# Optimization experiments

Measured on AMD Instinct MI355X. Metric: run time of the kernel, lower is better.

The kernel has to match this reference:

```python
import jax, jax.numpy as jnp
import numpy as np

CHUNK = 2048  # output-direction chunk size for the fused score+reduce scan


def _stereographic_normals(out_size):
    # matches torch.meshgrid default (ij indexing): v = rows, u = cols
    v, u = jnp.meshgrid(jnp.arange(out_size, dtype=jnp.float32),
                        jnp.arange(out_size, dtype=jnp.float32), indexing='ij')
    p = 4.0 * ((u + 0.5) / out_size - 0.5)
    q = -4.0 * ((v + 0.5) / out_size - 0.5)
    d = 1.0 + p ** 2 + q ** 2
    x = 2.0 * p / d
    y = 2.0 * q / d
    z = -(-1.0 + p ** 2 + q ** 2) / d
    return jnp.stack([x, y, z], axis=-1).reshape(-1, 3)  # [out_size^2, 3]


def _forward(image, normal_map, mask, kappa, out_size):
    B, C, H, W = image.shape
    N = H * W
    k = jnp.float32(kappa)
    coef = k / (2.0 * jnp.pi * (1.0 - jnp.exp(-2.0 * k)))  # vMF normalization

    V = image.reshape(B, C, N).transpose(0, 2, 1)              # [B,N,C]
    n_in = normal_map.reshape(B, 3, N).transpose(0, 2, 1)      # [B,N,3]
    w = (mask.reshape(B, N) > 0).astype(image.dtype)[..., None]  # 0/1 validity
    # fuse numerator (v^2) and denominator (v) accumulations into one pass
    Vaug = jnp.concatenate([V * w, (V ** 2) * w], axis=-1)     # [B,N,2C]

    M = _stereographic_normals(out_size)                        # [N_out,3]
    n_chunks = M.shape[0] // CHUNK
    chunks = M.reshape(n_chunks, CHUNK, 3)

    def body(carry, Mc):
        dp = jnp.einsum('bnd,cd->bnc', n_in, Mc)                # cos similarity
        f = coef * jnp.exp(-k * (1.0 - dp))                     # vMF kernel
        return carry, jnp.einsum('bnc,bnk->bck', f, Vaug)       # [B,CHUNK,2C]

    _, outs = jax.lax.scan(jax.checkpoint(body), 0.0, chunks)   # [n_chunks,B,CHUNK,2C]
    vals = outs.transpose(1, 0, 2, 3).reshape(B, out_size * out_size, 2 * C)
    s, num = vals[..., :C], vals[..., C:]
    out_pixels = num / (s + 0.001)                              # [B,N_out,C]
    return out_pixels.transpose(0, 2, 1).reshape(B, C, out_size, out_size)


def setup_inputs() -> dict:
    key = jax.random.key(0)
    k1, k2, k3 = jax.random.split(key, 3)
    B, C, H, W = 2, 3, 128, 128
    image = jax.random.uniform(k1, (B, C, H, W), dtype=jnp.float32)
    nm = jax.random.normal(k2, (B, 3, H, W), dtype=jnp.float32)
    nm = nm / jnp.linalg.norm(nm, axis=1, keepdims=True)  # unit normals
    mask = jax.random.randint(k3, (B, H, W), 0, 2).astype(jnp.int32)
    return {"image": image, "normal_map": nm, "mask": mask,
            "kappa": 100, "out_size": 256}


def reference(image, normal_map, mask, kappa, out_size):
    return _forward(image, normal_map, mask, kappa, out_size)
```

## Files before the change

### kernel.cpp

```cpp
#include <hip/hip_runtime.h>
#include <math.h>

#define B_     2
#define C_     3
#define N_     16384
#define OS_    256
#define OUT_   65536
#define NZ_    32
#define NF_    64
#define NB_    2048
#define NITEM_ 1536
#define GRIDM_ 2048
#define CAP_   16384
#define SP2_   256
#define VSTR_  264
#define TAU_   16.0f
#define LOG2E  1.44269504088896340736f
#define PI_    3.14159265358979323846f

typedef float    f32x4 __attribute__((ext_vector_type(4)));
typedef float    v2f   __attribute__((ext_vector_type(2)));
typedef _Float16 f16x8 __attribute__((ext_vector_type(8)));
typedef __fp16   h16x2 __attribute__((ext_vector_type(2)));

static __device__ __forceinline__ v2f pk_fma(v2f a, v2f b, v2f c) {
    return __builtin_elementwise_fma(a, b, c);
}

__device__ __forceinline__ int pixel_bin(float nx, float ny, float nz) {
    int zi = (int)((nz + 1.0f) * (NZ_ * 0.5f));
    zi = min(max(zi, 0), NZ_ - 1);
    float phi = atan2f(ny, nx);
    int fi = (int)((phi + PI_) * (NF_ / (2.0f * PI_)));
    fi = min(max(fi, 0), NF_ - 1);
    return zi * NF_ + fi;
}

__global__ __launch_bounds__(256) void hist_kernel(
    const float* __restrict__ nm, const int* __restrict__ mask, int* __restrict__ cnt)
{
    int idx = blockIdx.x * 256 + threadIdx.x;
    if (idx >= B_ * N_) return;
    if (mask[idx] <= 0) return;
    int b = idx / N_, n = idx - b * N_;
    const float* nb = nm + (size_t)b * 3 * N_ + n;
    int bin = pixel_bin(nb[0], nb[N_], nb[2 * N_]);
    atomicAdd(&cnt[b * NB_ + bin], 1);
}

__global__ __launch_bounds__(64) void scan_kernel(
    const int* __restrict__ cnt, int* __restrict__ binStart, int* __restrict__ off)
{
    int b = blockIdx.x;
    int lane = threadIdx.x;
    const int per = NB_ / 64;
    int base = b * NB_ + lane * per;

    int sum = 0;
#pragma unroll
    for (int i = 0; i < per; i++) sum += cnt[base + i];

    int inc = sum;
#pragma unroll
    for (int o = 1; o < 64; o <<= 1) {
        int t = __shfl_up(inc, o);
        if (lane >= o) inc += t;
    }
    int acc = inc - sum;

#pragma unroll
    for (int i = 0; i < per; i++) {
        binStart[b * (NB_ + 1) + lane * per + i] = acc;
        off[b * NB_ + lane * per + i] = acc;
        acc += cnt[base + i];
    }
    if (lane == 63) binStart[b * (NB_ + 1) + NB_] = acc;
}

__global__ __launch_bounds__(256) void scatter_plan_kernel(
    const float* __restrict__ img, const float* __restrict__ nm,
    const int* __restrict__ mask, const int* __restrict__ kappa,
    const int* __restrict__ binStart, int* __restrict__ off,
    float* __restrict__ gn, _Float16* __restrict__ gv,
    int* __restrict__ plan, int* __restrict__ tileLen)
{
    int tid = threadIdx.x;
    int bid = blockIdx.x;
    float k = (float)kappa[0];
    float k2 = k * LOG2E;

    if (bid < 128) {
        int idx = bid * 256 + tid;
        if (idx >= B_ * N_) return;
        if (mask[idx] <= 0) return;
        int b = idx / N_, n = idx - b * N_;
        const float* nb = nm + (size_t)b * 3 * N_ + n;
        float nx = nb[0], ny = nb[N_], nz = nb[2 * N_];
        int bin = pixel_bin(nx, ny, nz);
        int pos = atomicAdd(&off[b * NB_ + bin], 1);
        const float* ib = img + (size_t)b * C_ * N_ + n;
        float v0 = ib[0], v1 = ib[N_], v2 = ib[2 * N_];
        gn[((size_t)b * 3 + 0) * CAP_ + pos] = k2 * nx;
        gn[((size_t)b * 3 + 1) * CAP_ + pos] = k2 * ny;
        gn[((size_t)b * 3 + 2) * CAP_ + pos] = k2 * nz;
        _Float16* gvb = gv + (size_t)b * 6 * CAP_;
        gvb[0 * CAP_ + pos] = (_Float16)v0;
        gvb[1 * CAP_ + pos] = (_Float16)v1;
        gvb[2 * CAP_ + pos] = (_Float16)v2;
        gvb[3 * CAP_ + pos] = (_Float16)(v0 * v0);
        gvb[4 * CAP_ + pos] = (_Float16)(v1 * v1);
        gvb[5 * CAP_ + pos] = (_Float16)(v2 * v2);
        return;
    }

    __shared__ int warr[4];
    int bt = bid - 128;
    int b = bt >> 8, tile = bt & 255;
    int tu = tile & 15, tv = tile >> 4;
    int w = tid >> 6, lane = tid & 63;

    float pc  = 4.0f * ((tu * 16 + 8.0f) * (1.0f / OS_) - 0.5f);
    float qc  = -4.0f * ((tv * 16 + 8.0f) * (1.0f / OS_) - 0.5f);
    float ppc = pc * pc + qc * qc, invc = 1.0f / (1.0f + ppc);
    float Tx = 2.0f * pc * invc, Ty = 2.0f * qc * invc, Tz = (1.0f - ppc) * invc;

    float ctile = 1.0f;
#pragma unroll
    for (int j = 0; j < 4; j++) {
        int cl = j * 64 + lane;
        int u = tu * 16 + (cl & 15), v = tv * 16 + (cl >> 4);
        float p = 4.0f * ((u + 0.5f) * (1.0f / OS_) - 0.5f);
        float q = -4.0f * ((v + 0.5f) * (1.0f / OS_) - 0.5f);
        float pp = p * p + q * q;
        float inv = 1.0f / (1.0f + pp);
        float mx = 2.0f * p * inv, my = 2.0f * q * inv, mz = (1.0f - pp) * inv;
        ctile = fminf(ctile, mx * Tx + my * Ty + mz * Tz);
    }
#pragma unroll
    for (int o = 32; o; o >>= 1) ctile = fminf(ctile, __shfl_xor(ctile, o));

    float dpthr = fminf(fmaxf(1.0f - TAU_ / k, -1.0f), 1.0f);
    ctile = fminf(fmaxf(ctile, -1.0f), 1.0f);
    float theta = acosf(dpthr) + acosf(ctile);
    float rhs = (theta >= PI_) ? -2.0f : cosf(theta);

    float rT   = sqrtf(Tx * Tx + Ty * Ty);
    float phiT = atan2f(Ty, Tx);
    int fiT = min(max((int)((phiT + PI_) * (NF_ / (2.0f * PI_))), 0), NF_ - 1);

    const int* bs = binStart + b * (NB_ + 1);
    int Lacc = 0;

#pragma unroll
    for (int j = 0; j < 8; j++) {
        int zi = w + j * 4;
        float z0 = -1.0f + zi * (2.0f / NZ_);
        float z1 = z0 + (2.0f / NZ_);
        float hw  = PI_ / NF_;
        float mid = -PI_ + (2.0f * PI_ / NF_) * lane + hw;
        float d = phiT - mid;
        d = d - (2.0f * PI_) * rintf(d * (0.5f / PI_));
        d = fabsf(d);
        float cmax = (d <= hw) ? 1.0f : cosf(d - hw);
        float A  = rT * cmax;
        float g0 = A * sqrtf(fmaxf(0.0f, 1.0f - z0 * z0)) + Tz * z0;
        float g1 = A * sqrtf(fmaxf(0.0f, 1.0f - z1 * z1)) + Tz * z1;
        float gm = fmaxf(g0, g1);
        if (A > 0.0f) {
            float s2 = A * A + Tz * Tz;
            float zs = Tz * rsqrtf(s2);
            if (zs > z0 && zs < z1) gm = sqrtf(s2);
        }
        unsigned long long m = __ballot(gm >= rhs);

        int base = zi * NF_;
        int st0 = 0, en0 = 0, st1 = 0, en1 = 0;
        if (m) {
            bool full = (~m == 0ull) || !((m >> fiT) & 1ull);
            if (!full) {
                unsigned long long r = fiT ? ((m >> fiT) | (m << (64 - fiT))) : m;
                unsigned long long nr = ~r;
                int bcnt = __builtin_ctzll(nr);
                int acnt = __builtin_clzll(nr);
                if (bcnt + acnt >= NF_) full = true;
                else {
                    int lo = fiT - acnt, hi = fiT + bcnt - 1;
                    if (lo >= 0 && hi < NF_) {
                        st0 = bs[base + lo]; en0 = bs[base + hi + 1];
                    } else if (lo < 0) {
                        st0 = bs[base];            en0 = bs[base + hi + 1];
                        st1 = bs[base + lo + NF_]; en1 = bs[base + NF_];
                    } else {
                        st0 = bs[base];       en0 = bs[base + hi - NF_ + 1];
                        st1 = bs[base + lo];  en1 = bs[base + NF_];
                    }
                }
            }
            if (full) { st0 = bs[base]; en0 = bs[base + NF_]; }
        }
        Lacc += (en0 - st0) + (en1 - st1);
        if (lane == 0) {
            int* o = plan + ((size_t)bt * NZ_ + zi) * 4;
            o[0] = st0; o[1] = en0; o[2] = st1; o[3] = en1;
        }
    }
    if (lane == 0) warr[w] = Lacc;
    __syncthreads();
    if (tid == 0) tileLen[bt] = warr[0] + warr[1] + warr[2] + warr[3];
}

__global__ __launch_bounds__(256) void builder_kernel(
    const int* __restrict__ tileLen, int* __restrict__ tileItemStart,
    int* __restrict__ items, int* __restrict__ hdr)
{
    __shared__ int lds[256];
    int t = threadIdx.x;
    int bt0 = t * 2, bt1 = t * 2 + 1;
    int L0 = tileLen[bt0], L1 = tileLen[bt1];

    lds[t] = L0 + L1;
    __syncthreads();
    for (int o = 128; o > 0; o >>= 1) {
        if (t < o) lds[t] += lds[t + o];
        __syncthreads();
    }
    int SL = lds[0];
    __syncthreads();

    int R = (SL + NITEM_ - 1) / NITEM_;
    if (R < 32) R = 32;

    int P0 = (L0 + R - 1) / R, P1 = (L1 + R - 1) / R;
    int ps = P0 + P1;
    lds[t] = ps;
    __syncthreads();
    for (int o = 1; o < 256; o <<= 1) {
        int v = (t >= o) ? lds[t - o] : 0;
        __syncthreads();
        lds[t] += v;
        __syncthreads();
    }
    int excl  = lds[t] - ps;
    int total = lds[255];

    tileItemStart[bt0] = excl;
    tileItemStart[bt1] = excl + P0;
    if (t == 255) tileItemStart[512] = total;
    if (t == 0)   hdr[0] = R;

    for (int p = 0; p < P0; p++) items[excl + p]      = (bt0 << 12) | p;
    for (int p = 0; p < P1; p++) items[excl + P0 + p] = (bt1 << 12) | p;
    for (int i = total + t; i < GRIDM_; i += 256) items[i] = -1;
}

__global__ __launch_bounds__(256) void main_kernel(
    const float* __restrict__ gn, const _Float16* __restrict__ gv,
    const int* __restrict__ plan, const int* __restrict__ items,
    const int* __restrict__ hdr, const int* __restrict__ kappa,
    float* __restrict__ part2)
{
    __shared__ float    s_nx[SP2_], s_ny[SP2_], s_nz[SP2_];
    __shared__ _Float16 s_va[6 * VSTR_ + 8];
    __shared__ int      rTab[128];
    __shared__ int      gmap[SP2_];
    __shared__ int      sTot;

    int item = items[blockIdx.x];
    if (item < 0) return;
    int bt = item >> 12, piece = item & 4095;
    int tile = bt & 255, b = bt >> 8;
    int tu = tile & 15, tv = tile >> 4;
    int tid = threadIdx.x, w = tid >> 6, lane = tid & 63;

    if (tid < 64) {
        int st = plan[(size_t)bt * (NZ_ * 4) + 2 * tid];
        int en = plan[(size_t)bt * (NZ_ * 4) + 2 * tid + 1];
        int len = en - st; if (len < 0) len = 0;
        int inc = len;
#pragma unroll
        for (int o = 1; o < 64; o <<= 1) {
            int t2 = __shfl_up(inc, o);
            if (tid >= o) inc += t2;
        }
        int pos = inc - len;
        rTab[tid * 2]     = pos;
        rTab[tid * 2 + 1] = st - pos;
        if (tid == 63) sTot = inc;
    }
    if (tid >= 64 && tid < 72) s_va[6 * VSTR_ + (tid - 64)] = (_Float16)0.0f;
    __syncthreads();

    int R   = hdr[0];
    int tot = sTot;
    int plo = piece * R;
    int phi = min(tot, plo + R);

    float k2 = (float)kappa[0] * LOG2E;
    v2f mk2v = {-k2, -k2};

    v2f Mx2[4], My2[4], Mz2[4];
#pragma unroll
    for (int t = 0; t < 4; t++) {
        int u = tu * 16 + (lane & 15);
        int v = tv * 16 + w * 4 + t;
        float p  = 4.0f * ((u + 0.5f) * (1.0f / OS_) - 0.5f);
        float q  = -4.0f * ((v + 0.5f) * (1.0f / OS_) - 0.5f);
        float pp = p * p + q * q;
        float inv = 1.0f / (1.0f + pp);
        float mx = 2.0f * p * inv, my = 2.0f * q * inv, mz = (1.0f - pp) * inv;
        Mx2[t] = (v2f){mx, mx}; My2[t] = (v2f){my, my}; Mz2[t] = (v2f){mz, mz};
    }

    f32x4 acc[4];
#pragma unroll
    for (int t = 0; t < 4; t++) acc[t] = (f32x4){0.0f, 0.0f, 0.0f, 0.0f};

    const float* gnx = gn + ((size_t)b * 3 + 0) * CAP_;
    const float* gny = gn + ((size_t)b * 3 + 1) * CAP_;
    const float* gnz = gn + ((size_t)b * 3 + 2) * CAP_;
    const _Float16* gvb = gv + (size_t)b * 6 * CAP_;

    int ch   = lane & 15;
    int kgrp = (lane >> 4) * 8;

    for (int s0 = plo; s0 < phi; s0 += SP2_) {
        int sp  = min(SP2_, phi - s0);
        int spP = (sp + 31) & ~31;
        if (tid < sp) {
            int cp = s0 + tid, r = 0;
#pragma unroll
            for (int step = 32; step; step >>= 1) {
                int nr = r + step;
                if (rTab[nr * 2] <= cp) r = nr;
            }
            gmap[tid] = cp + rTab[r * 2 + 1];
        }
        __syncthreads();
        if (tid < sp) {
            int g = gmap[tid];
            s_nx[tid] = gnx[g]; s_ny[tid] = gny[g]; s_nz[tid] = gnz[g];
#pragma unroll
            for (int c2 = 0; c2 < 6; c2++) s_va[c2 * VSTR_ + tid] = gvb[c2 * CAP_ + g];
        } else if (tid < spP) {
            s_nx[tid] = 0.0f; s_ny[tid] = 0.0f; s_nz[tid] = 0.0f;
#pragma unroll
            for (int c2 = 0; c2 < 6; c2++) s_va[c2 * VSTR_ + tid] = (_Float16)0.0f;
        }
        __syncthreads();

        for (int k0 = 0; k0 < spP; k0 += 32) {
            int kr = k0 + kgrp;
            const v2f* xv = (const v2f*)&s_nx[kr];
            const v2f* yv = (const v2f*)&s_ny[kr];
            const v2f* zv = (const v2f*)&s_nz[kr];
            v2f x01 = xv[0], x23 = xv[1], x45 = xv[2], x67 = xv[3];
            v2f y01 = yv[0], y23 = yv[1], y45 = yv[2], y67 = yv[3];
            v2f z01 = zv[0], z23 = zv[1], z45 = zv[2], z67 = zv[3];
            f16x8 bfrag;
            if (ch < 6) bfrag = *(const f16x8*)&s_va[ch * VSTR_ + kr];
            else        bfrag = *(const f16x8*)&s_va[6 * VSTR_];
#pragma unroll
            for (int t = 0; t < 4; t++) {
                v2f g01 = pk_fma(x01, Mx2[t], pk_fma(y01, My2[t], pk_fma(z01, Mz2[t], mk2v)));
                v2f g23 = pk_fma(x23, Mx2[t], pk_fma(y23, My2[t], pk_fma(z23, Mz2[t], mk2v)));
                v2f g45 = pk_fma(x45, Mx2[t], pk_fma(y45, My2[t], pk_fma(z45, Mz2[t], mk2v)));
                v2f g67 = pk_fma(x67, Mx2[t], pk_fma(y67, My2[t], pk_fma(z67, Mz2[t], mk2v)));
                h16x2 p0 = __builtin_amdgcn_cvt_pkrtz(__builtin_amdgcn_exp2f(g01.x),
                                                      __builtin_amdgcn_exp2f(g01.y));
                h16x2 p1 = __builtin_amdgcn_cvt_pkrtz(__builtin_amdgcn_exp2f(g23.x),
                                                      __builtin_amdgcn_exp2f(g23.y));
                h16x2 p2 = __builtin_amdgcn_cvt_pkrtz(__builtin_amdgcn_exp2f(g45.x),
                                                      __builtin_amdgcn_exp2f(g45.y));
                h16x2 p3 = __builtin_amdgcn_cvt_pkrtz(__builtin_amdgcn_exp2f(g67.x),
                                                      __builtin_amdgcn_exp2f(g67.y));
                f16x8 afrag;
                afrag[0] = (_Float16)p0[0]; afrag[1] = (_Float16)p0[1];
                afrag[2] = (_Float16)p1[0]; afrag[3] = (_Float16)p1[1];
                afrag[4] = (_Float16)p2[0]; afrag[5] = (_Float16)p2[1];
                afrag[6] = (_Float16)p3[0]; afrag[7] = (_Float16)p3[1];
                acc[t] = __builtin_amdgcn_mfma_f32_16x16x32_f16(afrag, bfrag, acc[t], 0, 0, 0);
            }
        }
        __syncthreads();
    }

    if (ch < 6) {
        float* dst = part2 + (size_t)blockIdx.x * 1536;
#pragma unroll
        for (int t = 0; t < 4; t++) {
#pragma unroll
            for (int r = 0; r < 4; r++) {
                int d = w * 64 + t * 16 + ((lane >> 4) * 4 + r);
                dst[d * 6 + ch] = acc[t][r];
            }
        }
    }
}

__global__ __launch_bounds__(256) void finalize_kernel(
    const float* __restrict__ part2, const int* __restrict__ tileItemStart,
    const int* __restrict__ kappa, float* __restrict__ out)
{
    int idx = blockIdx.x * 256 + threadIdx.x;
    if (idx >= B_ * OUT_) return;
    int b = idx / OUT_;
    int c = idx - b * OUT_;
    int u = c & 255, v = c >> 8;
    int bt = b * 256 + ((v >> 4) * 16 + (u >> 4));
    int cl = (v & 15) * 16 + (u & 15);

    float k = (float)kappa[0];
    float coef = k / (2.0f * PI_ * (1.0f - expf(-2.0f * k)));

    int is0 = tileItemStart[bt], is1 = tileItemStart[bt + 1];
    float s[6] = {0, 0, 0, 0, 0, 0};
    for (int it = is0; it < is1; it++) {
        const float* p = part2 + (size_t)it * 1536 + cl * 6;
#pragma unroll
        for (int i = 0; i < 6; i++) s[i] += p[i];
    }
#pragma unroll
    for (int ch = 0; ch < C_; ch++) {
        out[((size_t)(b * C_ + ch)) * OUT_ + c] = (coef * s[3 + ch]) / (coef * s[ch] + 0.001f);
    }
}

extern "C" void kernel_launch(void* const* d_in, const int* in_sizes, int n_in,
                              void* d_out, int out_size, void* d_ws, size_t ws_size,
                              hipStream_t stream)
{
    const float* img   = (const float*)d_in[0];
    const float* nm    = (const float*)d_in[1];
    const int*   mask  = (const int*)d_in[2];
    const int*   kappa = (const int*)d_in[3];
    float* out = (float*)d_out;

    char* ws = (char*)d_ws;
    size_t o = 0;
    float*     gn        = (float*)(ws + o);     o += (size_t)B_ * 3 * CAP_ * 4;
    _Float16*  gv        = (_Float16*)(ws + o); o += (size_t)B_ * 6 * CAP_ * 2;
    float*     part2     = (float*)(ws + o);     o += (size_t)GRIDM_ * 1536 * 4;
    int* plan            = (int*)(ws + o);       o += (size_t)512 * NZ_ * 4 * 4;
    int* cnt             = (int*)(ws + o);       o += (size_t)B_ * NB_ * 4;
    int* off             = (int*)(ws + o);       o += (size_t)B_ * NB_ * 4;
    int* binStart        = (int*)(ws + o);       o += ((size_t)B_ * (NB_ + 1) * 4 + 15) & ~15ull;
    int* tileLen         = (int*)(ws + o);       o += 512 * 4;
    int* tileItemStart   = (int*)(ws + o);       o += (513 * 4 + 15) & ~15ull;
    int* items           = (int*)(ws + o);       o += GRIDM_ * 4;
    int* hdr             = (int*)(ws + o);       o += 16;

    (void)hipMemsetAsync(cnt, 0, (size_t)B_ * NB_ * sizeof(int), stream);
    hipLaunchKernelGGL(hist_kernel, dim3((B_ * N_ + 255) / 256), dim3(256), 0, stream,
                       nm, mask, cnt);
    hipLaunchKernelGGL(scan_kernel, dim3(B_), dim3(64), 0, stream,
                       cnt, binStart, off);
    hipLaunchKernelGGL(scatter_plan_kernel, dim3(640), dim3(256), 0, stream,
                       img, nm, mask, kappa, binStart, off, gn, gv, plan, tileLen);
    hipLaunchKernelGGL(builder_kernel, dim3(1), dim3(256), 0, stream,
                       tileLen, tileItemStart, items, hdr);
    hipLaunchKernelGGL(main_kernel, dim3(GRIDM_), dim3(256), 0, stream,
                       gn, gv, plan, items, hdr, kappa, part2);
    hipLaunchKernelGGL(finalize_kernel, dim3((B_ * OUT_ + 255) / 256), dim3(256), 0, stream,
                       part2, tileItemStart, kappa, out);
}
```

Measured before the change: 64.41 us.

## Fuse histogram and scan into one LDS kernel, lower kernel cutoff tau

Replaces the memset, the global-atomic histogram kernel and the scan kernel with a single kernel per batch. It builds the bin histogram in shared memory with 1024 threads and then scans it in place, which removes one memset and one launch along with the global atomics. Separately it lowers the TAU cutoff from 16 to 12, which likely shrinks the angular neighbourhood of bins processed per output tile. That reduces main-kernel work but drops more of the vMF kernel tail, so accuracy is lower. The fused histogram runs on only 2 blocks, so that stage has far less parallelism.

```diff
diff --git a/kernel.cpp b/kernel.cpp
--- a/kernel.cpp
+++ b/kernel.cpp
@@ -14,7 +14,7 @@
 #define CAP_   16384
 #define SP2_   256
 #define VSTR_  264
-#define TAU_   16.0f
+#define TAU_   12.0f
 #define LOG2E  1.44269504088896340736f
 #define PI_    3.14159265358979323846f
 
@@ -36,29 +36,35 @@
     return zi * NF_ + fi;
 }
 
-__global__ __launch_bounds__(256) void hist_kernel(
-    const float* __restrict__ nm, const int* __restrict__ mask, int* __restrict__ cnt)
-{
-    int idx = blockIdx.x * 256 + threadIdx.x;
-    if (idx >= B_ * N_) return;
-    if (mask[idx] <= 0) return;
-    int b = idx / N_, n = idx - b * N_;
-    const float* nb = nm + (size_t)b * 3 * N_ + n;
-    int bin = pixel_bin(nb[0], nb[N_], nb[2 * N_]);
-    atomicAdd(&cnt[b * NB_ + bin], 1);
-}
-
-__global__ __launch_bounds__(64) void scan_kernel(
-    const int* __restrict__ cnt, int* __restrict__ binStart, int* __restrict__ off)
-{
+__global__ __launch_bounds__(1024) void hist_scan_kernel(
+    const float* __restrict__ nm, const int* __restrict__ mask,
+    int* __restrict__ binStart, int* __restrict__ off)
+{
+    __shared__ int hist[NB_];
     int b = blockIdx.x;
-    int lane = threadIdx.x;
+    int tid = threadIdx.x;
+
+    for (int i = tid; i < NB_; i += 1024) hist[i] = 0;
+    __syncthreads();
+
+#pragma unroll
+    for (int j = 0; j < N_ / 1024; j++) {
+        int n = j * 1024 + tid;
+        if (mask[b * N_ + n] > 0) {
+            const float* nb = nm + (size_t)b * 3 * N_ + n;
+            atomicAdd(&hist[pixel_bin(nb[0], nb[N_], nb[2 * N_])], 1);
+        }
+    }
+    __syncthreads();
+
+    if (tid >= 64) return;
+    int lane = tid;
     const int per = NB_ / 64;
-    int base = b * NB_ + lane * per;
+    int base = lane * per;
 
     int sum = 0;
 #pragma unroll
-    for (int i = 0; i < per; i++) sum += cnt[base + i];
+    for (int i = 0; i < per; i++) sum += hist[base + i];
 
     int inc = sum;
 #pragma unroll
@@ -70,9 +76,9 @@
 
 #pragma unroll
     for (int i = 0; i < per; i++) {
-        binStart[b * (NB_ + 1) + lane * per + i] = acc;
-        off[b * NB_ + lane * per + i] = acc;
-        acc += cnt[base + i];
+        binStart[b * (NB_ + 1) + base + i] = acc;
+        off[b * NB_ + base + i] = acc;
+        acc += hist[base + i];
     }
     if (lane == 63) binStart[b * (NB_ + 1) + NB_] = acc;
 }
@@ -441,7 +447,6 @@
     _Float16*  gv        = (_Float16*)(ws + o); o += (size_t)B_ * 6 * CAP_ * 2;
     float*     part2     = (float*)(ws + o);     o += (size_t)GRIDM_ * 1536 * 4;
     int* plan            = (int*)(ws + o);       o += (size_t)512 * NZ_ * 4 * 4;
-    int* cnt             = (int*)(ws + o);       o += (size_t)B_ * NB_ * 4;
     int* off             = (int*)(ws + o);       o += (size_t)B_ * NB_ * 4;
     int* binStart        = (int*)(ws + o);       o += ((size_t)B_ * (NB_ + 1) * 4 + 15) & ~15ull;
     int* tileLen         = (int*)(ws + o);       o += 512 * 4;
@@ -449,11 +454,8 @@
     int* items           = (int*)(ws + o);       o += GRIDM_ * 4;
     int* hdr             = (int*)(ws + o);       o += 16;
 
-    (void)hipMemsetAsync(cnt, 0, (size_t)B_ * NB_ * sizeof(int), stream);
-    hipLaunchKernelGGL(hist_kernel, dim3((B_ * N_ + 255) / 256), dim3(256), 0, stream,
-                       nm, mask, cnt);
-    hipLaunchKernelGGL(scan_kernel, dim3(B_), dim3(64), 0, stream,
-                       cnt, binStart, off);
+    hipLaunchKernelGGL(hist_scan_kernel, dim3(B_), dim3(1024), 0, stream,
+                       nm, mask, binStart, off);
     hipLaunchKernelGGL(scatter_plan_kernel, dim3(640), dim3(256), 0, stream,
                        img, nm, mask, kappa, binStart, off, gn, gv, plan, tileLen);
     hipLaunchKernelGGL(builder_kernel, dim3(1), dim3(256), 0, stream,
```

After: 62.88 us. 2.4% less time.
